# Performance work log

Measured on AMD Instinct MI355X. Metric: run time of the kernel, lower is better.

Reference implementation:

```python
import jax, jax.numpy as jnp
import numpy as np

NUM_HEADS = 8
KEY_SIZE = 64
VALUE_SIZE = 64
NUM_GROUPS = 3 * NUM_HEADS  # 24
C = NUM_HEADS * (2 * KEY_SIZE + VALUE_SIZE)  # 1536
EPS = 1e-5


def setup_inputs() -> dict:
    key = jax.random.key(0)
    k1, k2, k3 = jax.random.split(key, 3)
    x = jax.random.normal(k1, (8, C, 32, 32), dtype=jnp.float32)
    # GroupNorm affine params (torch default ones/zeros, perturbed for non-trivial grads)
    gn_weight = 1.0 + 0.1 * jax.random.normal(k2, (C,), dtype=jnp.float32)
    gn_bias = 0.1 * jax.random.normal(k3, (C,), dtype=jnp.float32)
    return {"x": x, "gn_weight": gn_weight, "gn_bias": gn_bias}


def _group_norm(x, weight, bias):
    B, Cc, H, W = x.shape
    xg = x.reshape(B, NUM_GROUPS, -1)  # [B, G, (C/G)*H*W]
    mean = jnp.mean(xg, axis=-1, keepdims=True)
    var = jnp.var(xg, axis=-1, keepdims=True)
    xn = ((xg - mean) * jax.lax.rsqrt(var + EPS)).reshape(B, Cc, H, W)
    return xn * weight[:, None, None] + bias[:, None, None]


def reference(x, gn_weight, gn_bias):
    NH, KS, VS = NUM_HEADS, KEY_SIZE, VALUE_SIZE
    B, Cc, H, W = x.shape
    xn = _group_norm(x, gn_weight, gn_bias)
    xr = xn.reshape(B, NH, 2 * KS + VS, H * W)  # [B, NH, 2KS+VS, NK]
    k = xr[:, :, :KS]            # [B, NH, KS, NK]
    q = xr[:, :, KS:2 * KS]      # [B, NH, KS, NK]
    v = xr[:, :, 2 * KS:]        # [B, NH, VS, NK]
    # saliency = q^T @ k / sqrt(KS) -> [B, NH, NKq, NKk]
    sal = jnp.einsum('bhcq,bhck->bhqk', q, k) / jnp.sqrt(jnp.float32(KS))
    mask = jax.nn.softmax(sal, axis=-1)
    # out = v @ mask^T -> [B, NH, VS, NKq]
    out = jnp.einsum('bhvk,bhqk->bhvq', v, mask)
    return out.reshape(B, NH * VS, H, W)
```

## Files before the change

kernel.cpp:

```cpp
#include <hip/hip_runtime.h>
#include <hip/hip_bf16.h>


typedef __attribute__((ext_vector_type(8))) short bf16x8;
typedef __attribute__((ext_vector_type(4))) float f32x4;
typedef unsigned short u16;
typedef unsigned int u32;

#define SM_SCALE 0.18033688f
#define SM_OFF   8.0f

__device__ __forceinline__ u32 pack2(float a, float b) {
    union { float f; u32 u; } ua, ub; ua.f = a; ub.f = b;
    return __builtin_amdgcn_perm(ub.u + 0x8000u, ua.u + 0x8000u, 0x07060302u);
}
union BB { uint4 u; bf16x8 v; };

__global__ __launch_bounds__(256) void gn_partial(const float* __restrict__ x,
                                                  float* __restrict__ partials) {
    int blk = blockIdx.x;
    const float4* p = (const float4*)(x + (size_t)blk * 8192);
    int t = threadIdx.x;
    float s1a = 0.f, s2a = 0.f, s1b = 0.f, s2b = 0.f;
#pragma unroll
    for (int i = 0; i < 8; i += 2) {
        float4 va = p[t + i * 256];
        float4 vb = p[t + (i + 1) * 256];
        s1a += va.x + va.y + va.z + va.w;
        s2a += va.x*va.x + va.y*va.y + va.z*va.z + va.w*va.w;
        s1b += vb.x + vb.y + vb.z + vb.w;
        s2b += vb.x*vb.x + vb.y*vb.y + vb.z*vb.z + vb.w*vb.w;
    }
    float s1 = s1a + s1b, s2 = s2a + s2b;
    for (int off = 32; off > 0; off >>= 1) {
        s1 += __shfl_down(s1, off);
        s2 += __shfl_down(s2, off);
    }
    __shared__ float a1[4], a2[4];
    int wave = t >> 6, lane = t & 63;
    if (lane == 0) { a1[wave] = s1; a2[wave] = s2; }
    __syncthreads();
    if (t == 0) {
        partials[blk * 2 + 0] = a1[0] + a1[1] + a1[2] + a1[3];
        partials[blk * 2 + 1] = a2[0] + a2[1] + a2[2] + a2[3];
    }
}

__device__ __forceinline__ void group_stats(const float* __restrict__ partials,
                                            int bg, float& mean, float& rstd) {
    float s1 = 0.f, s2 = 0.f;
#pragma unroll
    for (int j = 0; j < 8; ++j) {
        s1 += partials[(bg * 8 + j) * 2 + 0];
        s2 += partials[(bg * 8 + j) * 2 + 1];
    }
    mean = s1 * (1.f / 65536.f);
    float var = s2 * (1.f / 65536.f) - mean * mean;
    rstd = rsqrtf(var + 1e-5f);
}

__global__ __launch_bounds__(256) void pack_kernel(
    const float* __restrict__ x, const float* __restrict__ gamma,
    const float* __restrict__ beta, const float* __restrict__ partials,
    u16* __restrict__ Qn, u16* __restrict__ Kn, u16* __restrict__ Vn)
{
    const int st = blockIdx.x >> 6, pair = blockIdx.x & 63;
    const int b = pair >> 3, h = pair & 7;
    const float* xb = x + (size_t)b * 1536 * 1024;
    float ms[3], rs[3];
    group_stats(partials, b * 24 + 3 * h + 0, ms[0], rs[0]);
    group_stats(partials, b * 24 + 3 * h + 1, ms[1], rs[1]);
    group_stats(partials, b * 24 + 3 * h + 2, ms[2], rs[2]);

    const int t = threadIdx.x;
    __shared__ u32 Tsh[64][33];

    const int cp = t >> 4;
    const int s4 = (t & 15) * 4;
    const int sgl = st * 64 + s4;

    for (int t2 = 0; t2 < 2; ++t2) {
        if (t2) __syncthreads();
#pragma unroll
        for (int dc = 0; dc < 2; ++dc) {
            int cg0 = h * 192 + t2 * 64 + dc * 32 + cp * 2;
            float4 va = *(const float4*)(xb + (size_t)cg0 * 1024 + sgl);
            float4 vb = *(const float4*)(xb + (size_t)(cg0 + 1) * 1024 + sgl);
            float w0 = gamma[cg0] * rs[t2],     b0 = beta[cg0] - ms[t2] * w0;
            float w1 = gamma[cg0 + 1] * rs[t2], b1 = beta[cg0 + 1] - ms[t2] * w1;
            int col = dc * 16 + cp;
            Tsh[s4 + 0][col] = pack2(va.x * w0 + b0, vb.x * w1 + b1);
            Tsh[s4 + 1][col] = pack2(va.y * w0 + b0, vb.y * w1 + b1);
            Tsh[s4 + 2][col] = pack2(va.z * w0 + b0, vb.z * w1 + b1);
            Tsh[s4 + 3][col] = pack2(va.w * w0 + b0, vb.w * w1 + b1);
        }
        __syncthreads();
        u16* dst = (t2 ? Qn : Kn) + (size_t)pair * 65536 + (size_t)st * 64 * 64;
#pragma unroll
        for (int p = 0; p < 2; ++p) {
            int row = p * 32 + (t >> 3);
            int c8 = (t & 7) * 4;
            uint4 o;
            o.x = Tsh[row][c8 + 0]; o.y = Tsh[row][c8 + 1];
            o.z = Tsh[row][c8 + 2]; o.w = Tsh[row][c8 + 3];
            *(uint4*)(dst + (size_t)row * 64 + c8 * 2) = o;
        }
    }
    {
#pragma unroll
        for (int dc = 0; dc < 4; ++dc) {
            int c = dc * 16 + (t >> 4);
            int cg = h * 192 + 128 + c;
            float4 v = *(const float4*)(xb + (size_t)cg * 1024 + sgl);
            float wsc = gamma[cg] * rs[2];
            float bsc = beta[cg] - ms[2] * wsc;
            uint2 o;
            o.x = pack2(v.x * wsc + bsc, v.y * wsc + bsc);
            o.y = pack2(v.z * wsc + bsc, v.w * wsc + bsc);
            *(uint2*)(Vn + (size_t)pair * 65536 + (size_t)c * 1024 + sgl) = o;
        }
    }
}

__global__ __launch_bounds__(256, 2) void attn_kernel(
    const u16* __restrict__ Qn, const u16* __restrict__ Kn,
    const u16* __restrict__ Vn, float* __restrict__ out)
{
    const int bid = blockIdx.x;
    const int qt = bid >> 6;
    const int pair = bid & 63;
    const int tid = threadIdx.x;
    const int w = tid >> 6;
    const int lane = tid & 63;
    const int grp = lane >> 4, li = lane & 15;

    __shared__ uint4 KT[2][512];
    __shared__ uint4 VT[2][512];
    __shared__ u32 PT[4][2][16][36];

    const u16* Qp = Qn + (size_t)pair * 65536;
    const u16* Kp = Kn + (size_t)pair * 65536;
    const u16* Vp = Vn + (size_t)pair * 65536;

    const int j0 = tid * 2;
    const int srow = j0 >> 3;
    const int sch  = j0 & 7;
    const int sx   = srow & 7;
    const int idx0 = srow * 8 + (sch ^ sx);
    const int idx1 = srow * 8 + ((sch + 1) ^ sx);

    const int q0 = qt * 128 + w * 32;
    bf16x8 bq[2][2];
#pragma unroll
    for (int qf = 0; qf < 2; ++qf) {
        const u16* qrow = Qp + (size_t)(q0 + qf * 16 + li) * 64 + grp * 8;
        bq[qf][0] = *(const bf16x8*)(qrow);
        bq[qf][1] = *(const bf16x8*)(qrow + 32);
    }

    f32x4 oacc[2][4];
#pragma unroll
    for (int qf = 0; qf < 2; ++qf)
#pragma unroll
        for (int vf = 0; vf < 4; ++vf) oacc[qf][vf] = f32x4{0.f, 0.f, 0.f, 0.f};
    float lsum[2] = {0.f, 0.f};

    u32* const prow0 = &PT[w][0][li][0];
    u32* const prow1 = &PT[w][1][li][0];
    const int g1 = (2 * grp) & 3, g2 = (2 * grp + 1) & 3;
    const int koff = 2 * (grp >> 1);

    uint4 s0, s1, s2, s3;
    s0 = *(const uint4*)(Kp + (size_t)j0 * 8);
    s1 = *(const uint4*)(Kp + (size_t)j0 * 8 + 8);
    s2 = *(const uint4*)(Vp + (size_t)srow * 1024 + sch * 8);
    s3 = *(const uint4*)(Vp + (size_t)srow * 1024 + sch * 8 + 8);
    KT[0][idx0] = s0; KT[0][idx1] = s1;
    VT[0][idx0] = s2; VT[0][idx1] = s3;
    __syncthreads();

#pragma unroll 2
    for (int kt = 0; kt < 16; ++kt) {
        const int cur = kt & 1;
        if (kt < 15) {
            s0 = *(const uint4*)(Kp + (size_t)(kt + 1) * 4096 + j0 * 8);
            s1 = *(const uint4*)(Kp + (size_t)(kt + 1) * 4096 + j0 * 8 + 8);
            s2 = *(const uint4*)(Vp + (size_t)srow * 1024 + (kt + 1) * 64 + sch * 8);
            s3 = *(const uint4*)(Vp + (size_t)srow * 1024 + (kt + 1) * 64 + sch * 8 + 8);
        }

        const int x7 = li & 7;
        bf16x8 ak[4][2];
#pragma unroll
        for (int kf = 0; kf < 4; ++kf) {
            const int rb = (kf * 16 + li) * 8;
            ak[kf][0] = ((const BB*)&KT[cur][rb + ((0 + grp) ^ x7)])->v;
            ak[kf][1] = ((const BB*)&KT[cur][rb + ((4 + grp) ^ x7)])->v;
        }
        f32x4 sf[2][4];
#pragma unroll
        for (int qf = 0; qf < 2; ++qf)
#pragma unroll
            for (int kf = 0; kf < 4; ++kf) {
                f32x4 acc = f32x4{0.f, 0.f, 0.f, 0.f};
                acc = __builtin_amdgcn_mfma_f32_16x16x32_bf16(ak[kf][0], bq[qf][0], acc, 0, 0, 0);
                acc = __builtin_amdgcn_mfma_f32_16x16x32_bf16(ak[kf][1], bq[qf][1], acc, 0, 0, 0);
                sf[qf][kf] = acc;
            }
#pragma unroll
        for (int qf = 0; qf < 2; ++qf) {
            u32 pr[8];
#pragma unroll
            for (int kf = 0; kf < 4; ++kf) {
                float p0 = exp2f(__builtin_fmaf(sf[qf][kf][0], SM_SCALE, -SM_OFF));
                float p1 = exp2f(__builtin_fmaf(sf[qf][kf][1], SM_SCALE, -SM_OFF));
                float p2 = exp2f(__builtin_fmaf(sf[qf][kf][2], SM_SCALE, -SM_OFF));
                float p3 = exp2f(__builtin_fmaf(sf[qf][kf][3], SM_SCALE, -SM_OFF));
                lsum[qf] += (p0 + p1) + (p2 + p3);
                pr[kf * 2 + 0] = pack2(p0, p1);
                pr[kf * 2 + 1] = pack2(p2, p3);
            }
            u32* pw = (qf ? prow1 : prow0) + grp * 8;
            *(uint4*)(pw + 0) = uint4{pr[0], pr[1], pr[2], pr[3]};
            *(uint4*)(pw + 4) = uint4{pr[4], pr[5], pr[6], pr[7]};
        }
        bf16x8 av[4][2];
#pragma unroll
        for (int vf = 0; vf < 4; ++vf) {
            const int rb = (vf * 16 + li) * 8;
            av[vf][0] = ((const BB*)&VT[cur][rb + ((0 + grp) ^ x7)])->v;
            av[vf][1] = ((const BB*)&VT[cur][rb + ((4 + grp) ^ x7)])->v;
        }
#pragma unroll
        for (int qf = 0; qf < 2; ++qf) {
            const u32* rp = qf ? prow1 : prow0;
#pragma unroll
            for (int kh = 0; kh < 2; ++kh) {
                uint2 a = *(const uint2*)(rp + g1 * 8 + 4 * kh + koff);
                uint2 b = *(const uint2*)(rp + g2 * 8 + 4 * kh + koff);
                BB pb; pb.u = uint4{a.x, a.y, b.x, b.y};
#pragma unroll
                for (int vf = 0; vf < 4; ++vf)
                    oacc[qf][vf] = __builtin_amdgcn_mfma_f32_16x16x32_bf16(av[vf][kh], pb.v, oacc[qf][vf], 0, 0, 0);
            }
        }
        if (kt < 15) {
            const int nxt = cur ^ 1;
            KT[nxt][idx0] = s0; KT[nxt][idx1] = s1;
            VT[nxt][idx0] = s2; VT[nxt][idx1] = s3;
        }
        __syncthreads();
    }

#pragma unroll
    for (int qf = 0; qf < 2; ++qf) {
        lsum[qf] += __shfl_xor(lsum[qf], 16);
        lsum[qf] += __shfl_xor(lsum[qf], 32);
        float invl = 1.f / lsum[qf];
        float* ob = out + (size_t)pair * 65536 + q0 + qf * 16 + li;
#pragma unroll
        for (int vf = 0; vf < 4; ++vf)
#pragma unroll
            for (int r = 0; r < 4; ++r) {
                int v = vf * 16 + grp * 4 + r;
                ob[(size_t)v * 1024] = oacc[qf][vf][r] * invl;
            }
    }
}

extern "C" void kernel_launch(void* const* d_in, const int* in_sizes, int n_in,
                              void* d_out, int out_size, void* d_ws, size_t ws_size,
                              hipStream_t stream) {
    const float* x     = (const float*)d_in[0];
    const float* gamma = (const float*)d_in[1];
    const float* beta  = (const float*)d_in[2];
    float* out = (float*)d_out;

    float* partials = (float*)d_ws;
    u16* Qn = (u16*)((char*)d_ws + 32768);
    u16* Kn = Qn + (size_t)64 * 65536;
    u16* Vn = Kn + (size_t)64 * 65536;

    gn_partial<<<1536, 256, 0, stream>>>(x, partials);
    pack_kernel<<<1024, 256, 0, stream>>>(x, gamma, beta, partials, Qn, Kn, Vn);
    attn_kernel<<<512, 256, 0, stream>>>(Qn, Kn, Vn, out);
}
```

Measured before the change: 134.5 us.

## Switch attention to 32x32x16 MFMA and pass P via permlane swap

Rewrites the attention kernel's QK^T and PV products to use 32x32x16 bf16 MFMA tiles instead of 16x16x32, with each wave owning a 32-query tile. The softmax probabilities are repacked in registers using permlane32 swaps, falling back to shuffles, rather than round-tripping through a per-wave LDS buffer. The MFMA blocks are also wrapped in s_setprio. This is meant to cut LDS traffic and instruction count per tile and raise matrix-core utilisation. It relies on the 32x32 accumulator lane layout being mapped correctly onto the B-operand layout.

```diff
diff --git a/kernel.cpp b/kernel.cpp
--- a/kernel.cpp
+++ b/kernel.cpp
@@ -4,6 +4,7 @@
 
 typedef __attribute__((ext_vector_type(8))) short bf16x8;
 typedef __attribute__((ext_vector_type(4))) float f32x4;
+typedef __attribute__((ext_vector_type(16))) float f32x16;
 typedef unsigned short u16;
 typedef unsigned int u32;
 
@@ -15,6 +16,25 @@
     return __builtin_amdgcn_perm(ub.u + 0x8000u, ua.u + 0x8000u, 0x07060302u);
 }
 union BB { uint4 u; bf16x8 v; };
+
+__device__ __forceinline__ f32x16 zero16() {
+    f32x16 z;
+#pragma unroll
+    for (int i = 0; i < 16; ++i) z[i] = 0.f;
+    return z;
+}
+
+__device__ __forceinline__ void swap32(u32 a, u32 b, int hi, u32& ret0, u32& ret1) {
+#if __has_builtin(__builtin_amdgcn_permlane32_swap)
+    (void)hi;
+    auto sw = __builtin_amdgcn_permlane32_swap(a, b, false, false);
+    ret0 = sw[0]; ret1 = sw[1];
+#else
+    u32 pa = __shfl_xor(a, 32), pb = __shfl_xor(b, 32);
+    ret0 = hi ? pb : a;
+    ret1 = hi ? b : pa;
+#endif
+}
 
 __global__ __launch_bounds__(256) void gn_partial(const float* __restrict__ x,
                                                   float* __restrict__ partials) {
@@ -132,11 +152,11 @@
     const int tid = threadIdx.x;
     const int w = tid >> 6;
     const int lane = tid & 63;
-    const int grp = lane >> 4, li = lane & 15;
+    const int li = lane & 31;
+    const int hi = lane >> 5;
 
     __shared__ uint4 KT[2][512];
     __shared__ uint4 VT[2][512];
-    __shared__ u32 PT[4][2][16][36];
 
     const u16* Qp = Qn + (size_t)pair * 65536;
     const u16* Kp = Kn + (size_t)pair * 65536;
@@ -150,25 +170,16 @@
     const int idx1 = srow * 8 + ((sch + 1) ^ sx);
 
     const int q0 = qt * 128 + w * 32;
-    bf16x8 bq[2][2];
-#pragma unroll
-    for (int qf = 0; qf < 2; ++qf) {
-        const u16* qrow = Qp + (size_t)(q0 + qf * 16 + li) * 64 + grp * 8;
-        bq[qf][0] = *(const bf16x8*)(qrow);
-        bq[qf][1] = *(const bf16x8*)(qrow + 32);
-    }
-
-    f32x4 oacc[2][4];
-#pragma unroll
-    for (int qf = 0; qf < 2; ++qf)
-#pragma unroll
-        for (int vf = 0; vf < 4; ++vf) oacc[qf][vf] = f32x4{0.f, 0.f, 0.f, 0.f};
-    float lsum[2] = {0.f, 0.f};
-
-    u32* const prow0 = &PT[w][0][li][0];
-    u32* const prow1 = &PT[w][1][li][0];
-    const int g1 = (2 * grp) & 3, g2 = (2 * grp + 1) & 3;
-    const int koff = 2 * (grp >> 1);
+    bf16x8 bq[4];
+#pragma unroll
+    for (int cs = 0; cs < 4; ++cs)
+        bq[cs] = *(const bf16x8*)(Qp + (size_t)(q0 + li) * 64 + cs * 16 + hi * 8);
+
+    f32x16 oacc[2];
+    oacc[0] = zero16(); oacc[1] = zero16();
+    float lsum = 0.f;
+
+    const int x7 = li & 7;
 
     uint4 s0, s1, s2, s3;
     s0 = *(const uint4*)(Kp + (size_t)j0 * 8);
@@ -189,61 +200,57 @@
             s3 = *(const uint4*)(Vp + (size_t)srow * 1024 + (kt + 1) * 64 + sch * 8 + 8);
         }
 
-        const int x7 = li & 7;
-        bf16x8 ak[4][2];
-#pragma unroll
-        for (int kf = 0; kf < 4; ++kf) {
-            const int rb = (kf * 16 + li) * 8;
-            ak[kf][0] = ((const BB*)&KT[cur][rb + ((0 + grp) ^ x7)])->v;
-            ak[kf][1] = ((const BB*)&KT[cur][rb + ((4 + grp) ^ x7)])->v;
-        }
-        f32x4 sf[2][4];
-#pragma unroll
-        for (int qf = 0; qf < 2; ++qf)
-#pragma unroll
-            for (int kf = 0; kf < 4; ++kf) {
-                f32x4 acc = f32x4{0.f, 0.f, 0.f, 0.f};
-                acc = __builtin_amdgcn_mfma_f32_16x16x32_bf16(ak[kf][0], bq[qf][0], acc, 0, 0, 0);
-                acc = __builtin_amdgcn_mfma_f32_16x16x32_bf16(ak[kf][1], bq[qf][1], acc, 0, 0, 0);
-                sf[qf][kf] = acc;
+        f32x16 sf[2];
+#pragma unroll
+        for (int kf = 0; kf < 2; ++kf) {
+            bf16x8 ak[4];
+#pragma unroll
+            for (int cs = 0; cs < 4; ++cs)
+                ak[cs] = ((const BB*)&KT[cur][(kf * 32 + li) * 8 + ((cs * 2 + hi) ^ x7)])->v;
+            f32x16 acc = zero16();
+            __builtin_amdgcn_s_setprio(1);
+#pragma unroll
+            for (int cs = 0; cs < 4; ++cs)
+                acc = __builtin_amdgcn_mfma_f32_32x32x16_bf16(ak[cs], bq[cs], acc, 0, 0, 0);
+            __builtin_amdgcn_s_setprio(0);
+            sf[kf] = acc;
+        }
+
+        BB pbv[4];
+#pragma unroll
+        for (int kf = 0; kf < 2; ++kf)
+#pragma unroll
+            for (int s = 0; s < 2; ++s) {
+                float p0 = exp2f(__builtin_fmaf(sf[kf][8 * s + 0], SM_SCALE, -SM_OFF));
+                float p1 = exp2f(__builtin_fmaf(sf[kf][8 * s + 1], SM_SCALE, -SM_OFF));
+                float p2 = exp2f(__builtin_fmaf(sf[kf][8 * s + 2], SM_SCALE, -SM_OFF));
+                float p3 = exp2f(__builtin_fmaf(sf[kf][8 * s + 3], SM_SCALE, -SM_OFF));
+                float p4 = exp2f(__builtin_fmaf(sf[kf][8 * s + 4], SM_SCALE, -SM_OFF));
+                float p5 = exp2f(__builtin_fmaf(sf[kf][8 * s + 5], SM_SCALE, -SM_OFF));
+                float p6 = exp2f(__builtin_fmaf(sf[kf][8 * s + 6], SM_SCALE, -SM_OFF));
+                float p7 = exp2f(__builtin_fmaf(sf[kf][8 * s + 7], SM_SCALE, -SM_OFF));
+                lsum += ((p0 + p1) + (p2 + p3)) + ((p4 + p5) + (p6 + p7));
+                u32 Pa = pack2(p0, p1), Pb = pack2(p2, p3);
+                u32 Pc = pack2(p4, p5), Pd = pack2(p6, p7);
+                u32 w0, w1, w2, w3;
+                swap32(Pa, Pc, hi, w0, w2);
+                swap32(Pb, Pd, hi, w1, w3);
+                pbv[kf * 2 + s].u = uint4{w0, w1, w2, w3};
             }
-#pragma unroll
-        for (int qf = 0; qf < 2; ++qf) {
-            u32 pr[8];
-#pragma unroll
-            for (int kf = 0; kf < 4; ++kf) {
-                float p0 = exp2f(__builtin_fmaf(sf[qf][kf][0], SM_SCALE, -SM_OFF));
-                float p1 = exp2f(__builtin_fmaf(sf[qf][kf][1], SM_SCALE, -SM_OFF));
-                float p2 = exp2f(__builtin_fmaf(sf[qf][kf][2], SM_SCALE, -SM_OFF));
-                float p3 = exp2f(__builtin_fmaf(sf[qf][kf][3], SM_SCALE, -SM_OFF));
-                lsum[qf] += (p0 + p1) + (p2 + p3);
-                pr[kf * 2 + 0] = pack2(p0, p1);
-                pr[kf * 2 + 1] = pack2(p2, p3);
-            }
-            u32* pw = (qf ? prow1 : prow0) + grp * 8;
-            *(uint4*)(pw + 0) = uint4{pr[0], pr[1], pr[2], pr[3]};
-            *(uint4*)(pw + 4) = uint4{pr[4], pr[5], pr[6], pr[7]};
-        }
-        bf16x8 av[4][2];
-#pragma unroll
-        for (int vf = 0; vf < 4; ++vf) {
-            const int rb = (vf * 16 + li) * 8;
-            av[vf][0] = ((const BB*)&VT[cur][rb + ((0 + grp) ^ x7)])->v;
-            av[vf][1] = ((const BB*)&VT[cur][rb + ((4 + grp) ^ x7)])->v;
-        }
-#pragma unroll
-        for (int qf = 0; qf < 2; ++qf) {
-            const u32* rp = qf ? prow1 : prow0;
-#pragma unroll
-            for (int kh = 0; kh < 2; ++kh) {
-                uint2 a = *(const uint2*)(rp + g1 * 8 + 4 * kh + koff);
-                uint2 b = *(const uint2*)(rp + g2 * 8 + 4 * kh + koff);
-                BB pb; pb.u = uint4{a.x, a.y, b.x, b.y};
-#pragma unroll
-                for (int vf = 0; vf < 4; ++vf)
-                    oacc[qf][vf] = __builtin_amdgcn_mfma_f32_16x16x32_bf16(av[vf][kh], pb.v, oacc[qf][vf], 0, 0, 0);
-            }
-        }
+
+#pragma unroll
+        for (int vf = 0; vf < 2; ++vf) {
+            bf16x8 av[4];
+#pragma unroll
+            for (int ks = 0; ks < 4; ++ks)
+                av[ks] = ((const BB*)&VT[cur][(vf * 32 + li) * 8 + ((ks * 2 + hi) ^ x7)])->v;
+            __builtin_amdgcn_s_setprio(1);
+#pragma unroll
+            for (int ks = 0; ks < 4; ++ks)
+                oacc[vf] = __builtin_amdgcn_mfma_f32_32x32x16_bf16(av[ks], pbv[ks].v, oacc[vf], 0, 0, 0);
+            __builtin_amdgcn_s_setprio(0);
+        }
+
         if (kt < 15) {
             const int nxt = cur ^ 1;
             KT[nxt][idx0] = s0; KT[nxt][idx1] = s1;
@@ -252,20 +259,16 @@
         __syncthreads();
     }
 
-#pragma unroll
-    for (int qf = 0; qf < 2; ++qf) {
-        lsum[qf] += __shfl_xor(lsum[qf], 16);
-        lsum[qf] += __shfl_xor(lsum[qf], 32);
-        float invl = 1.f / lsum[qf];
-        float* ob = out + (size_t)pair * 65536 + q0 + qf * 16 + li;
-#pragma unroll
-        for (int vf = 0; vf < 4; ++vf)
-#pragma unroll
-            for (int r = 0; r < 4; ++r) {
-                int v = vf * 16 + grp * 4 + r;
-                ob[(size_t)v * 1024] = oacc[qf][vf][r] * invl;
-            }
-    }
+    lsum += __shfl_xor(lsum, 32);
+    float invl = 1.f / lsum;
+    float* ob = out + (size_t)pair * 65536 + q0 + li;
+#pragma unroll
+    for (int vf = 0; vf < 2; ++vf)
+#pragma unroll
+        for (int r = 0; r < 16; ++r) {
+            int v = vf * 32 + (r & 3) + 8 * (r >> 2) + 4 * hi;
+            ob[(size_t)v * 1024] = oacc[vf][r] * invl;
+        }
 }
 
 extern "C" void kernel_launch(void* const* d_in, const int* in_sizes, int n_in,
```

Result: faster. 131.6 us (-2.2%).
